# Kernel optimization log

Hardware: AMD Instinct MI355X
Metric: run time of the kernel (lower is better)

## Reference

```python
import jax, jax.numpy as jnp
import numpy as np

IMAGE_SIZE = 224
BLUR_SIGMA = 4.0  # PIL ImageFilter.GaussianBlur(radius=4): radius acts as std dev
BLUR_RADIUS = 8   # truncate kernel at 2*sigma


def _gaussian_blur(x, sigma=BLUR_SIGMA, radius=BLUR_RADIUS):
    # separable gaussian blur on NCHW, SAME padding
    t = jnp.arange(-radius, radius + 1, dtype=x.dtype)
    kern = jnp.exp(-0.5 * (t / sigma) ** 2)
    kern = kern / kern.sum()
    dn = ('NCHW', 'OIHW', 'NCHW')
    x = jax.lax.conv_general_dilated(x, kern.reshape(1, 1, 1, -1), (1, 1), 'SAME', dimension_numbers=dn)
    x = jax.lax.conv_general_dilated(x, kern.reshape(1, 1, -1, 1), (1, 1), 'SAME', dimension_numbers=dn)
    return x


def setup_inputs() -> dict:
    key = jax.random.key(0)
    ks = jax.random.split(key, 8)
    N = 1000
    inp = {
        'z': jax.random.normal(ks[0], (1, 512), jnp.float32),
        'fmap0': jax.random.normal(ks[1], (1, 64, 56, 56), jnp.float32),
        'fmap1': jax.random.normal(ks[2], (1, 128, 28, 28), jnp.float32),
        'fmap2': jax.random.normal(ks[3], (1, 256, 14, 14), jnp.float32),
        'z_lib': jax.random.normal(ks[4], (N, 512), jnp.float32),
        'lib0': jax.random.normal(ks[5], (N, 64, 56, 56), jnp.float32),
        'lib1': jax.random.normal(ks[6], (N, 128, 28, 28), jnp.float32),
        'lib2': jax.random.normal(ks[7], (N, 256, 14, 14), jnp.float32),
        'k': 5,
    }
    return inp


def reference(z, fmap0, fmap1, fmap2, z_lib, lib0, lib1, lib2, k):
    # distances = ||z_lib - z||_2 over feature dim -> [N]
    dists = jnp.linalg.norm(z_lib - z, axis=1)
    # topk smallest
    neg_vals, indices = jax.lax.top_k(-dists, k)
    z_score = (-neg_vals).mean()

    s_total = jnp.zeros((1, 1, IMAGE_SIZE, IMAGE_SIZE), jnp.float32)
    for fmap, lib in ((fmap0, lib0), (fmap1, lib1), (fmap2, lib2)):
        nearest = lib[indices]                            # [k, C, H, W]
        s = jnp.linalg.norm(nearest - fmap, axis=1)        # [k, H, W] (channel-wise L2)
        s = s.min(axis=0, keepdims=True)                   # [1, H, W]
        s_up = jax.image.resize(s[None], (1, 1, IMAGE_SIZE, IMAGE_SIZE), method='bilinear')
        s_total = s_total + s_up
    s_total = _gaussian_blur(s_total)
    return z_score, s_total
```

## Files before the change

kernel.cpp:

```cpp
#include <hip/hip_runtime.h>
#include <hip/hip_bf16.h>
#include <math.h>

#define IMG 224
#define NLIB 1000
#define ZD 512
#define MAXK 8
#define NTHR 512
#define STHR 256
#define SBLK 172


__device__ __forceinline__ int clampk(int k) {
    if (k < 1) k = 1;
    if (k > MAXK) k = MAXK;
    return k;
}

__global__ void __launch_bounds__(NTHR) k_dist(const float* __restrict__ z,
                                               const float* __restrict__ zlib,
                                               float* __restrict__ dists) {
    int lane = threadIdx.x & 63, wave = threadIdx.x >> 6;
    int gw = blockIdx.x * (NTHR / 64) + wave;
    if (gw >= NLIB) return;
    const float4* row4 = (const float4*)(zlib + (size_t)gw * ZD);
    const float4* z4   = (const float4*)z;
    float4 a0 = row4[lane],      b0 = z4[lane];
    float4 a1 = row4[64 + lane], b1 = z4[64 + lane];
    float acc = 0.f, d;
    d = a0.x - b0.x; acc += d * d;  d = a0.y - b0.y; acc += d * d;
    d = a0.z - b0.z; acc += d * d;  d = a0.w - b0.w; acc += d * d;
    d = a1.x - b1.x; acc += d * d;  d = a1.y - b1.y; acc += d * d;
    d = a1.z - b1.z; acc += d * d;  d = a1.w - b1.w; acc += d * d;
#pragma unroll
    for (int off = 32; off > 0; off >>= 1) acc += __shfl_xor(acc, off, 64);
    if (lane == 0) dists[gw] = sqrtf(acc);
}

__global__ void __launch_bounds__(STHR) k_score(
        const float* __restrict__ f0, const float* __restrict__ f1,
        const float* __restrict__ f2,
        const float* __restrict__ l0, const float* __restrict__ l1,
        const float* __restrict__ l2,
        const float* __restrict__ dists, const int* __restrict__ kp,
        float* __restrict__ out,
        float* __restrict__ s0, float* __restrict__ s1, float* __restrict__ s2) {

    int tid = threadIdx.x;
    int lane = tid & 63, wv = tid >> 6;
    int k = clampk(*kp);

    int n0 = k * 1568, n1 = k * 784, n2 = k * 392;
    int njobs = n0 + n1 + n2;
    int nwj = (njobs + 63) >> 6;
    int s = blockIdx.x + SBLK * wv;
    bool wvalid = (s < nwj);
    bool scorer = (blockIdx.x == 0 && wv == 0);
    if (!wvalid && !scorer) return;

    float vals[16];
#pragma unroll
    for (int q = 0; q < 16; ++q) {
        int e = lane + 64 * q;
        vals[q] = (e < NLIB) ? dists[e] : 3.4e38f;
    }
    int idxr[8];
    float ssum = 0.f;
#pragma unroll
    for (int it = 0; it < 8; ++it) {
        if (it < k) {
            float bv = 3.4e38f; int bi = 0x7fffffff;
#pragma unroll
            for (int q = 0; q < 16; ++q) {
                if (vals[q] < bv) { bv = vals[q]; bi = lane + 64 * q; }
            }
#pragma unroll
            for (int off = 1; off < 64; off <<= 1) {
                float ov = __shfl_xor(bv, off, 64);
                int   oi = __shfl_xor(bi, off, 64);
                if (ov < bv || (ov == bv && oi < bi)) { bv = ov; bi = oi; }
            }
#pragma unroll
            for (int q = 0; q < 16; ++q) {
                if (lane + 64 * q == bi) vals[q] = 3.4e38f;
            }
            idxr[it] = bi; ssum += bv;
        } else {
            idxr[it] = 0;
        }
    }
    if (scorer && lane == 0) out[0] = ssum / (float)k;
    if (!wvalid) return;

    int j = s * 64 + lane;
    if (j >= njobs) return;

    const float* fmp; const float* lbp; float* op;
    int kk, pq, cbase, HW, Cfull;
    if (j < n0) {
        int r = j;           kk = r / 1568; int q = r % 1568;
        int part = q / 784;  pq = q % 784;  cbase = part * 32;
        HW = 3136; Cfull = 64;  fmp = f0; lbp = l0;
        op = s0 + part * (MAXK * 3136) + kk * 3136;
    } else if (j < n0 + n1) {
        int r = j - n0;      kk = r / 784;  int q = r % 784;
        int part = q / 196;  pq = q % 196;  cbase = part * 32;
        HW = 784;  Cfull = 128; fmp = f1; lbp = l1;
        op = s1 + part * (MAXK * 784) + kk * 784;
    } else {
        int r = j - n0 - n1; kk = r / 392;  int q = r % 392;
        int part = q / 49;   pq = q % 49;   cbase = part * 32;
        HW = 196;  Cfull = 256; fmp = f2; lbp = l2;
        op = s2 + part * (MAXK * 196) + kk * 196;
    }
    int myidx = 0;
#pragma unroll
    for (int it = 0; it < 8; ++it) if (it == kk) myidx = idxr[it];

    const float4* lb4 = (const float4*)(lbp + (size_t)myidx * (size_t)Cfull * HW
                                            + (size_t)cbase * HW);
    const float4* fb4 = (const float4*)(fmp + (size_t)cbase * HW);
    int HW4 = HW >> 2;
    float ax = 0.f, ay = 0.f, az = 0.f, aw = 0.f;
#pragma unroll
    for (int c = 0; c < 32; ++c) {
        float4 a = lb4[c * HW4 + pq];
        float4 b = fb4[c * HW4 + pq];
        float dx = a.x - b.x, dy = a.y - b.y, dz = a.z - b.z, dw = a.w - b.w;
        ax += dx * dx; ay += dy * dy; az += dz * dz; aw += dw * dw;
    }
    float4 r; r.x = ax; r.y = ay; r.z = az; r.w = aw;
    ((float4*)op)[pq] = r;
}

__device__ __forceinline__ float bilin(const float* __restrict__ msm, int Wl, int Win,
                                       int bx, int by, float scl, int gx, int gy) {
    float sxf = ((float)gx + 0.5f) * scl - 0.5f;
    float syf = ((float)gy + 0.5f) * scl - 0.5f;
    float fx = floorf(sxf), fy = floorf(syf);
    float wx = sxf - fx,    wy = syf - fy;
    int ix = (int)fx, iy = (int)fy;
    int x0c = min(max(ix, 0), Win - 1) - bx, x1c = min(max(ix + 1, 0), Win - 1) - bx;
    int y0c = min(max(iy, 0), Win - 1) - by, y1c = min(max(iy + 1, 0), Win - 1) - by;
    float v00 = msm[y0c * Wl + x0c], v10 = msm[y0c * Wl + x1c];
    float v01 = msm[y1c * Wl + x0c], v11 = msm[y1c * Wl + x1c];
    return (1.f - wy) * ((1.f - wx) * v00 + wx * v10) +
           wy * ((1.f - wx) * v01 + wx * v11);
}

__global__ void __launch_bounds__(NTHR) k_tile(
        const float* __restrict__ s0, const float* __restrict__ s1,
        const float* __restrict__ s2, const int* __restrict__ kp,
        float* __restrict__ out) {

    __shared__ float msm0[100];
    __shared__ float msm1[36];
    __shared__ float msm2[9];
    __shared__ float pre[32 * 32];
    __shared__ float mid[32 * 16];
    __shared__ float wk[17];

    int tid = threadIdx.x;
    int k = clampk(*kp);
    int tx = blockIdx.x % 14, ty = blockIdx.x / 14;
    int x0 = tx * 16, y0 = ty * 16;
    int b0x = x0 / 4 - 3,  b0y = y0 / 4 - 3;
    int b1x = x0 / 8 - 2,  b1y = y0 / 8 - 2;
    int b2x = x0 / 16 - 1, b2y = y0 / 16 - 1;

    if (tid < 17) {
        float r = (float)(tid - 8) * 0.25f;
        wk[tid] = expf(-0.5f * r * r);
    }

    if (tid >= 64 && tid < 64 + 145) {
        int i = tid - 64;
        float m = 3.4e38f;
        if (i < 100) {
            int ly = i / 10, lx = i % 10;
            int gx = min(max(b0x + lx, 0), 55), gy = min(max(b0y + ly, 0), 55);
            int p = gy * 56 + gx;
            for (int kk = 0; kk < k; ++kk) {
                float v = s0[kk * 3136 + p] + s0[MAXK * 3136 + kk * 3136 + p];
                m = fminf(m, v);
            }
            msm0[i] = sqrtf(m);
        } else if (i < 136) {
            int r = i - 100; int ly = r / 6, lx = r % 6;
            int gx = min(max(b1x + lx, 0), 27), gy = min(max(b1y + ly, 0), 27);
            int p = gy * 28 + gx;
            for (int kk = 0; kk < k; ++kk) {
                float v = 0.f;
#pragma unroll
                for (int part = 0; part < 4; ++part)
                    v += s1[part * (MAXK * 784) + kk * 784 + p];
                m = fminf(m, v);
            }
            msm1[r] = sqrtf(m);
        } else {
            int r = i - 136; int ly = r / 3, lx = r % 3;
            int gx = min(max(b2x + lx, 0), 13), gy = min(max(b2y + ly, 0), 13);
            int p = gy * 14 + gx;
            for (int kk = 0; kk < k; ++kk) {
                float v = 0.f;
#pragma unroll
                for (int part = 0; part < 8; ++part)
                    v += s2[part * (MAXK * 196) + kk * 196 + p];
                m = fminf(m, v);
            }
            msm2[r] = sqrtf(m);
        }
    }
    __syncthreads();

    float wsum = 0.f;
#pragma unroll
    for (int t = 0; t < 17; ++t) wsum += wk[t];
    float inv2 = 1.f / (wsum * wsum);

    for (int i = tid; i < 32 * 32; i += NTHR) {
        int lx = i % 32, ly = i / 32;
        int gx = x0 - 8 + lx, gy = y0 - 8 + ly;
        float v = 0.f;
        if ((unsigned)gx < (unsigned)IMG && (unsigned)gy < (unsigned)IMG) {
            v = bilin(msm0, 10, 56, b0x, b0y, 0.25f,   gx, gy)
              + bilin(msm1, 6,  28, b1x, b1y, 0.125f,  gx, gy)
              + bilin(msm2, 3,  14, b2x, b2y, 0.0625f, gx, gy);
        }
        pre[i] = v;
    }
    __syncthreads();

    if (tid < 32 * 16) {
        int cx = tid % 16, ly = tid / 16;
        float acc = 0.f;
#pragma unroll
        for (int t = 0; t < 17; ++t) acc += wk[t] * pre[ly * 32 + cx + t];
        mid[ly * 16 + cx] = acc;
    }
    __syncthreads();

    if (tid < 16 * 16) {
        int ox = tid % 16, oy = tid / 16;
        float acc = 0.f;
#pragma unroll
        for (int t = 0; t < 17; ++t) acc += wk[t] * mid[(oy + t) * 16 + ox];
        out[1 + (y0 + oy) * IMG + (x0 + ox)] = acc * inv2;
    }
}

extern "C" void kernel_launch(void* const* d_in, const int* in_sizes, int n_in,
                              void* d_out, int out_size, void* d_ws, size_t ws_size,
                              hipStream_t stream) {
    const float* z    = (const float*)d_in[0];
    const float* f0   = (const float*)d_in[1];
    const float* f1   = (const float*)d_in[2];
    const float* f2   = (const float*)d_in[3];
    const float* zlib = (const float*)d_in[4];
    const float* l0   = (const float*)d_in[5];
    const float* l1   = (const float*)d_in[6];
    const float* l2   = (const float*)d_in[7];
    const int*   kp   = (const int*)d_in[8];
    float* out = (float*)d_out;

    float* ws    = (float*)d_ws;
    float* dists = ws;
    float* s0    = ws + 1024;
    float* s1    = s0 + 2 * MAXK * 3136;
    float* s2    = s1 + 4 * MAXK * 784;

    k_dist<<<(NLIB + 7) / 8, NTHR, 0, stream>>>(z, zlib, dists);
    k_score<<<SBLK, STHR, 0, stream>>>(f0, f1, f2, l0, l1, l2, dists, kp, out,
                                       s0, s1, s2);
    k_tile<<<196, NTHR, 0, stream>>>(s0, s1, s2, kp, out);
}
```

Before: 24.41 us.

## Merge score and tile kernels using flag-polled partial sums across blocks

Fuses the scoring kernel into the tile/blur kernel, saving one launch. The partial-sum buffer is prefilled with -1 by the distance kernel, and tile threads spin-poll with agent-scope atomic loads until the values they need become non-negative. This removes a kernel boundary and its launch gap, but it relies on every producer block being co-resident with the blocks that wait on it. A bounded spin guard keeps it from hanging forever, and the prefill adds extra stores to the first kernel.

```diff
diff --git a/kernel.cpp b/kernel.cpp
--- a/kernel.cpp
+++ b/kernel.cpp
@@ -7,9 +7,12 @@
 #define ZD 512
 #define MAXK 8
 #define NTHR 512
-#define STHR 256
-#define SBLK 172
-
+#define KA_BLK 125
+#define KB_BLK 196
+#define S0F (2 * MAXK * 3136)
+#define S1F (4 * MAXK * 784)
+#define S2F (8 * MAXK * 196)
+#define SFLOATS (S0F + S1F + S2F)
 
 __device__ __forceinline__ int clampk(int k) {
     if (k < 1) k = 1;
@@ -17,12 +20,23 @@
     return k;
 }
 
-__global__ void __launch_bounds__(NTHR) k_dist(const float* __restrict__ z,
-                                               const float* __restrict__ zlib,
-                                               float* __restrict__ dists) {
-    int lane = threadIdx.x & 63, wave = threadIdx.x >> 6;
-    int gw = blockIdx.x * (NTHR / 64) + wave;
-    if (gw >= NLIB) return;
+__device__ __forceinline__ void cgs_f32(float* p, float v) {
+    __hip_atomic_store(p, v, __ATOMIC_RELAXED, __HIP_MEMORY_SCOPE_AGENT);
+}
+__device__ __forceinline__ float cgl_f32(const float* p) {
+    return __hip_atomic_load((float*)p, __ATOMIC_RELAXED, __HIP_MEMORY_SCOPE_AGENT);
+}
+
+__global__ void __launch_bounds__(NTHR) k_pre(const float* __restrict__ z,
+                                              const float* __restrict__ zlib,
+                                              float* __restrict__ dists,
+                                              float* __restrict__ sfill) {
+    int tid = threadIdx.x, lane = tid & 63, wave = tid >> 6, bid = blockIdx.x;
+
+    for (int g = bid * NTHR + tid; g < SFLOATS; g += KA_BLK * NTHR)
+        cgs_f32(sfill + g, -1.0f);
+
+    int gw = bid * 8 + wave;
     const float4* row4 = (const float4*)(zlib + (size_t)gw * ZD);
     const float4* z4   = (const float4*)z;
     float4 a0 = row4[lane],      b0 = z4[lane];
@@ -37,100 +51,49 @@
     if (lane == 0) dists[gw] = sqrtf(acc);
 }
 
-__global__ void __launch_bounds__(STHR) k_score(
-        const float* __restrict__ f0, const float* __restrict__ f1,
-        const float* __restrict__ f2,
-        const float* __restrict__ l0, const float* __restrict__ l1,
-        const float* __restrict__ l2,
-        const float* __restrict__ dists, const int* __restrict__ kp,
-        float* __restrict__ out,
-        float* __restrict__ s0, float* __restrict__ s1, float* __restrict__ s2) {
-
-    int tid = threadIdx.x;
-    int lane = tid & 63, wv = tid >> 6;
-    int k = clampk(*kp);
-
-    int n0 = k * 1568, n1 = k * 784, n2 = k * 392;
-    int njobs = n0 + n1 + n2;
-    int nwj = (njobs + 63) >> 6;
-    int s = blockIdx.x + SBLK * wv;
-    bool wvalid = (s < nwj);
-    bool scorer = (blockIdx.x == 0 && wv == 0);
-    if (!wvalid && !scorer) return;
-
-    float vals[16];
-#pragma unroll
-    for (int q = 0; q < 16; ++q) {
-        int e = lane + 64 * q;
-        vals[q] = (e < NLIB) ? dists[e] : 3.4e38f;
-    }
-    int idxr[8];
-    float ssum = 0.f;
-#pragma unroll
-    for (int it = 0; it < 8; ++it) {
-        if (it < k) {
-            float bv = 3.4e38f; int bi = 0x7fffffff;
-#pragma unroll
-            for (int q = 0; q < 16; ++q) {
-                if (vals[q] < bv) { bv = vals[q]; bi = lane + 64 * q; }
-            }
-#pragma unroll
-            for (int off = 1; off < 64; off <<= 1) {
-                float ov = __shfl_xor(bv, off, 64);
-                int   oi = __shfl_xor(bi, off, 64);
-                if (ov < bv || (ov == bv && oi < bi)) { bv = ov; bi = oi; }
-            }
-#pragma unroll
-            for (int q = 0; q < 16; ++q) {
-                if (lane + 64 * q == bi) vals[q] = 3.4e38f;
-            }
-            idxr[it] = bi; ssum += bv;
-        } else {
-            idxr[it] = 0;
-        }
-    }
-    if (scorer && lane == 0) out[0] = ssum / (float)k;
-    if (!wvalid) return;
-
-    int j = s * 64 + lane;
-    if (j >= njobs) return;
-
-    const float* fmp; const float* lbp; float* op;
-    int kk, pq, cbase, HW, Cfull;
-    if (j < n0) {
-        int r = j;           kk = r / 1568; int q = r % 1568;
-        int part = q / 784;  pq = q % 784;  cbase = part * 32;
-        HW = 3136; Cfull = 64;  fmp = f0; lbp = l0;
-        op = s0 + part * (MAXK * 3136) + kk * 3136;
-    } else if (j < n0 + n1) {
-        int r = j - n0;      kk = r / 784;  int q = r % 784;
-        int part = q / 196;  pq = q % 196;  cbase = part * 32;
-        HW = 784;  Cfull = 128; fmp = f1; lbp = l1;
-        op = s1 + part * (MAXK * 784) + kk * 784;
-    } else {
-        int r = j - n0 - n1; kk = r / 392;  int q = r % 392;
-        int part = q / 49;   pq = q % 49;   cbase = part * 32;
-        HW = 196;  Cfull = 256; fmp = f2; lbp = l2;
-        op = s2 + part * (MAXK * 196) + kk * 196;
-    }
-    int myidx = 0;
-#pragma unroll
-    for (int it = 0; it < 8; ++it) if (it == kk) myidx = idxr[it];
-
-    const float4* lb4 = (const float4*)(lbp + (size_t)myidx * (size_t)Cfull * HW
-                                            + (size_t)cbase * HW);
-    const float4* fb4 = (const float4*)(fmp + (size_t)cbase * HW);
-    int HW4 = HW >> 2;
-    float ax = 0.f, ay = 0.f, az = 0.f, aw = 0.f;
-#pragma unroll
-    for (int c = 0; c < 32; ++c) {
-        float4 a = lb4[c * HW4 + pq];
-        float4 b = fb4[c * HW4 + pq];
-        float dx = a.x - b.x, dy = a.y - b.y, dz = a.z - b.z, dw = a.w - b.w;
-        ax += dx * dx; ay += dy * dy; az += dz * dz; aw += dw * dw;
-    }
-    float4 r; r.x = ax; r.y = ay; r.z = az; r.w = aw;
-    ((float4*)op)[pq] = r;
+template<int K, int P>
+__device__ float poll_min(const float* base, int strideK, int strideP, int pix) {
+    float v[K][P];
+    long guard = 0;
+    for (;;) {
+        bool ok = true;
+#pragma unroll
+        for (int kq = 0; kq < K; ++kq)
+#pragma unroll
+            for (int pp = 0; pp < P; ++pp)
+                v[kq][pp] = cgl_f32(base + (size_t)pp * strideP + kq * strideK + pix);
+#pragma unroll
+        for (int kq = 0; kq < K; ++kq)
+#pragma unroll
+            for (int pp = 0; pp < P; ++pp)
+                ok &= (v[kq][pp] >= 0.f);
+        if (ok) break;
+        if (++guard > 20000000L) break;
+        __builtin_amdgcn_s_sleep(1);
+    }
+    float m = 3.4e38f;
+#pragma unroll
+    for (int kq = 0; kq < K; ++kq) {
+        float s = 0.f;
+#pragma unroll
+        for (int pp = 0; pp < P; ++pp) s += v[kq][pp];
+        m = fminf(m, s);
+    }
+    return m;
+}
+
+template<int P>
+__device__ __forceinline__ float poll_min_k(int k, const float* base, int sK, int sP, int pix) {
+    switch (k) {
+        case 1: return poll_min<1, P>(base, sK, sP, pix);
+        case 2: return poll_min<2, P>(base, sK, sP, pix);
+        case 3: return poll_min<3, P>(base, sK, sP, pix);
+        case 4: return poll_min<4, P>(base, sK, sP, pix);
+        case 5: return poll_min<5, P>(base, sK, sP, pix);
+        case 6: return poll_min<6, P>(base, sK, sP, pix);
+        case 7: return poll_min<7, P>(base, sK, sP, pix);
+        default: return poll_min<8, P>(base, sK, sP, pix);
+    }
 }
 
 __device__ __forceinline__ float bilin(const float* __restrict__ msm, int Wl, int Win,
@@ -148,66 +111,135 @@
            wy * ((1.f - wx) * v01 + wx * v11);
 }
 
-__global__ void __launch_bounds__(NTHR) k_tile(
-        const float* __restrict__ s0, const float* __restrict__ s1,
-        const float* __restrict__ s2, const int* __restrict__ kp,
-        float* __restrict__ out) {
-
-    __shared__ float msm0[100];
-    __shared__ float msm1[36];
-    __shared__ float msm2[9];
+__global__ void __launch_bounds__(NTHR) k_main(
+        const float* __restrict__ f0, const float* __restrict__ f1,
+        const float* __restrict__ f2,
+        const float* __restrict__ l0, const float* __restrict__ l1,
+        const float* __restrict__ l2,
+        const float* __restrict__ dists, const int* __restrict__ kp,
+        float* __restrict__ out,
+        float* __restrict__ s0, float* __restrict__ s1, float* __restrict__ s2) {
+
+    __shared__ float msm0[100], msm1[36], msm2[9];
     __shared__ float pre[32 * 32];
     __shared__ float mid[32 * 16];
     __shared__ float wk[17];
 
-    int tid = threadIdx.x;
+    int tid = threadIdx.x, lane = tid & 63, wv = tid >> 6, bid = blockIdx.x;
     int k = clampk(*kp);
-    int tx = blockIdx.x % 14, ty = blockIdx.x / 14;
+
+    if (tid < 17) {
+        float r = (float)(tid - 8) * 0.25f;
+        wk[tid] = expf(-0.5f * r * r);
+    }
+
+    int tx = bid % 14, ty = bid / 14;
     int x0 = tx * 16, y0 = ty * 16;
     int b0x = x0 / 4 - 3,  b0y = y0 / 4 - 3;
     int b1x = x0 / 8 - 2,  b1y = y0 / 8 - 2;
     int b2x = x0 / 16 - 1, b2y = y0 / 16 - 1;
 
-    if (tid < 17) {
-        float r = (float)(tid - 8) * 0.25f;
-        wk[tid] = expf(-0.5f * r * r);
-    }
-
-    if (tid >= 64 && tid < 64 + 145) {
-        int i = tid - 64;
-        float m = 3.4e38f;
+    int n0 = k * 1568, n1 = k * 784, n2 = k * 392;
+    int njobs = n0 + n1 + n2;
+    int nwj = (njobs + 63) >> 6;
+    if (wv < 2) {
+        int s = bid + KB_BLK * wv;
+        bool havejob = (s < nwj);
+        bool scorer = (bid == 0 && wv == 0);
+        if (havejob || scorer) {
+            float vals[16];
+#pragma unroll
+            for (int q = 0; q < 16; ++q) {
+                int e = lane + 64 * q;
+                vals[q] = (e < NLIB) ? dists[e] : 3.4e38f;
+            }
+            int idxr[8];
+            float ssum = 0.f;
+#pragma unroll
+            for (int it = 0; it < 8; ++it) {
+                if (it < k) {
+                    float bv = 3.4e38f; int bi = 0x7fffffff;
+#pragma unroll
+                    for (int q = 0; q < 16; ++q) {
+                        if (vals[q] < bv) { bv = vals[q]; bi = lane + 64 * q; }
+                    }
+#pragma unroll
+                    for (int off = 1; off < 64; off <<= 1) {
+                        float ov = __shfl_xor(bv, off, 64);
+                        int   oi = __shfl_xor(bi, off, 64);
+                        if (ov < bv || (ov == bv && oi < bi)) { bv = ov; bi = oi; }
+                    }
+#pragma unroll
+                    for (int q = 0; q < 16; ++q) {
+                        if (lane + 64 * q == bi) vals[q] = 3.4e38f;
+                    }
+                    idxr[it] = bi; ssum += bv;
+                } else idxr[it] = 0;
+            }
+            if (scorer && lane == 0) out[0] = ssum / (float)k;
+
+            if (havejob) {
+                int j = s * 64 + lane;
+                if (j < njobs) {
+                    const float* fmp; const float* lbp; float* op;
+                    int kk, pq, cbase, HW, Cfull;
+                    if (j < n0) {
+                        int r = j;           kk = r / 1568; int q = r % 1568;
+                        int part = q / 784;  pq = q % 784;  cbase = part * 32;
+                        HW = 3136; Cfull = 64;  fmp = f0; lbp = l0;
+                        op = s0 + part * (MAXK * 3136) + kk * 3136;
+                    } else if (j < n0 + n1) {
+                        int r = j - n0;      kk = r / 784;  int q = r % 784;
+                        int part = q / 196;  pq = q % 196;  cbase = part * 32;
+                        HW = 784;  Cfull = 128; fmp = f1; lbp = l1;
+                        op = s1 + part * (MAXK * 784) + kk * 784;
+                    } else {
+                        int r = j - n0 - n1; kk = r / 392;  int q = r % 392;
+                        int part = q / 49;   pq = q % 49;   cbase = part * 32;
+                        HW = 196;  Cfull = 256; fmp = f2; lbp = l2;
+                        op = s2 + part * (MAXK * 196) + kk * 196;
+                    }
+                    int myidx = 0;
+#pragma unroll
+                    for (int it = 0; it < 8; ++it) if (it == kk) myidx = idxr[it];
+
+                    const float4* lb4 = (const float4*)(lbp + (size_t)myidx * (size_t)Cfull * HW
+                                                            + (size_t)cbase * HW);
+                    const float4* fb4 = (const float4*)(fmp + (size_t)cbase * HW);
+                    int HW4 = HW >> 2;
+                    float ax = 0.f, ay = 0.f, az = 0.f, aw = 0.f;
+#pragma unroll
+                    for (int c = 0; c < 32; ++c) {
+                        float4 a = lb4[c * HW4 + pq];
+                        float4 b = fb4[c * HW4 + pq];
+                        float dx = a.x - b.x, dy = a.y - b.y, dz = a.z - b.z, dw = a.w - b.w;
+                        ax += dx * dx; ay += dy * dy; az += dz * dz; aw += dw * dw;
+                    }
+                    float* o = op + 4 * pq;
+                    cgs_f32(o + 0, ax); cgs_f32(o + 1, ay);
+                    cgs_f32(o + 2, az); cgs_f32(o + 3, aw);
+                }
+            }
+        }
+    }
+
+    if (tid >= 128 && tid < 128 + 145) {
+        int i = tid - 128;
+        float m;
         if (i < 100) {
             int ly = i / 10, lx = i % 10;
             int gx = min(max(b0x + lx, 0), 55), gy = min(max(b0y + ly, 0), 55);
-            int p = gy * 56 + gx;
-            for (int kk = 0; kk < k; ++kk) {
-                float v = s0[kk * 3136 + p] + s0[MAXK * 3136 + kk * 3136 + p];
-                m = fminf(m, v);
-            }
+            m = poll_min_k<2>(k, s0, 3136, MAXK * 3136, gy * 56 + gx);
             msm0[i] = sqrtf(m);
         } else if (i < 136) {
             int r = i - 100; int ly = r / 6, lx = r % 6;
             int gx = min(max(b1x + lx, 0), 27), gy = min(max(b1y + ly, 0), 27);
-            int p = gy * 28 + gx;
-            for (int kk = 0; kk < k; ++kk) {
-                float v = 0.f;
-#pragma unroll
-                for (int part = 0; part < 4; ++part)
-                    v += s1[part * (MAXK * 784) + kk * 784 + p];
-                m = fminf(m, v);
-            }
+            m = poll_min_k<4>(k, s1, 784, MAXK * 784, gy * 28 + gx);
             msm1[r] = sqrtf(m);
         } else {
             int r = i - 136; int ly = r / 3, lx = r % 3;
             int gx = min(max(b2x + lx, 0), 13), gy = min(max(b2y + ly, 0), 13);
-            int p = gy * 14 + gx;
-            for (int kk = 0; kk < k; ++kk) {
-                float v = 0.f;
-#pragma unroll
-                for (int part = 0; part < 8; ++part)
-                    v += s2[part * (MAXK * 196) + kk * 196 + p];
-                m = fminf(m, v);
-            }
+            m = poll_min_k<8>(k, s2, 196, MAXK * 196, gy * 14 + gx);
             msm2[r] = sqrtf(m);
         }
     }
@@ -266,11 +298,10 @@
     float* ws    = (float*)d_ws;
     float* dists = ws;
     float* s0    = ws + 1024;
-    float* s1    = s0 + 2 * MAXK * 3136;
-    float* s2    = s1 + 4 * MAXK * 784;
-
-    k_dist<<<(NLIB + 7) / 8, NTHR, 0, stream>>>(z, zlib, dists);
-    k_score<<<SBLK, STHR, 0, stream>>>(f0, f1, f2, l0, l1, l2, dists, kp, out,
-                                       s0, s1, s2);
-    k_tile<<<196, NTHR, 0, stream>>>(s0, s1, s2, kp, out);
-}
+    float* s1    = s0 + S0F;
+    float* s2    = s1 + S1F;
+
+    k_pre<<<KA_BLK, NTHR, 0, stream>>>(z, zlib, dists, s0);
+    k_main<<<KB_BLK, NTHR, 0, stream>>>(f0, f1, f2, l0, l1, l2, dists, kp, out,
+                                        s0, s1, s2);
+}
```

Result: slower. 26.22 us (+7.4%).
